# Optimization experiments

Hardware: AMD Instinct MI355X
Metric: run time of the kernel (lower is better)

The kernel has to match this reference:

```python
import jax, jax.numpy as jnp
import numpy as np

N, E, G = 8000, 32000, 256   # nodes, edges, graphs
F, H = 680, 10               # in-features, GAT heads
HF = F * H                   # 6800


def setup_inputs() -> dict:
    key = jax.random.key(0)
    ks = jax.random.split(key, 12)
    s = lambda i, shape, sc: (jax.random.normal(ks[i], shape, jnp.float32) * sc)
    x = jax.random.normal(ks[0], (N, F), jnp.float32)
    edge_index = jax.random.randint(ks[1], (2, E), 0, N)
    batch = jnp.arange(N) // (N // G)   # contiguous, every graph non-empty
    return dict(
        x=x, edge_index=edge_index, batch=batch,
        W_gat=s(2, (F, HF), 0.05), a_src=s(3, (H, F), 0.05), a_dst=s(4, (H, F), 0.05),
        b_gat=jnp.zeros((HF,), jnp.float32),
        W_gcn=s(5, (HF, HF), 0.01), b_gcn=jnp.zeros((HF,), jnp.float32),
        W1=s(6, (2 * HF, 512), 0.02), b1=jnp.zeros((512,), jnp.float32),
        W2=s(7, (512, 128), 0.05), b2=jnp.zeros((128,), jnp.float32),
        W3=s(8, (128, 64), 0.05), b3=jnp.zeros((64,), jnp.float32),
    )


def _self_loops(edge_index):
    loop = jnp.arange(N)
    return (jnp.concatenate([edge_index[0], loop]),
            jnp.concatenate([edge_index[1], loop]))


def _gat(x, src, dst, W, a_s, a_d, b):
    xh = (x @ W).reshape(N, H, F)                          # [N,H,F]
    al_s = jnp.einsum('nhf,hf->nh', xh, a_s)               # src attention logits
    al_d = jnp.einsum('nhf,hf->nh', xh, a_d)
    e = jax.nn.leaky_relu(al_s[src] + al_d[dst], 0.2)      # [Etot,H]
    m = jax.ops.segment_max(e, dst, num_segments=N)        # segment softmax over dst
    ex = jnp.exp(e - m[dst])
    z = jax.ops.segment_sum(ex, dst, num_segments=N)
    alpha = ex / (z[dst] + 1e-16)
    out = jax.ops.segment_sum(alpha[:, :, None] * xh[src], dst, num_segments=N)
    return out.reshape(N, HF) + b                          # concat heads + bias


def _gcn(x, src, dst, W, b):
    deg = jax.ops.segment_sum(jnp.ones_like(dst, jnp.float32), dst, num_segments=N)
    dinv = jax.lax.rsqrt(deg)                              # deg>=1 due to self-loops
    norm = dinv[src] * dinv[dst]
    xw = x @ W
    return jax.ops.segment_sum(norm[:, None] * xw[src], dst, num_segments=N) + b


def reference(x, edge_index, batch, W_gat, a_src, a_dst, b_gat, W_gcn, b_gcn,
              W1, b1, W2, b2, W3, b3):
    src, dst = _self_loops(edge_index)
    h = jax.nn.relu(_gat(x, src, dst, W_gat, a_src, a_dst, b_gat))  # dropout = id (eval)
    h = jax.nn.relu(_gcn(h, src, dst, W_gcn, b_gcn))
    gmp = jax.ops.segment_max(h, batch, num_segments=G)
    cnt = jax.ops.segment_sum(jnp.ones((N,), jnp.float32), batch, num_segments=G)
    gap = jax.ops.segment_sum(h, batch, num_segments=G) / cnt[:, None]
    g = jnp.concatenate([gmp, gap], axis=1)                # [G, 2*HF]
    g = jax.nn.relu(g @ W1 + b1)
    g = g @ W2 + b2
    return g @ W3 + b3                                     # [G, 64]
```

## Files before the change

kernel.cpp:

```cpp
#include <hip/hip_runtime.h>
#include <cstdint>
#include <cstddef>

#define DEVFN static __device__ __forceinline__

typedef __attribute__((ext_vector_type(8))) short short8;
typedef __attribute__((ext_vector_type(16))) float f32x16;

constexpr int NN  = 8000;
constexpr int NE  = 32000;
constexpr int ET  = NE + NN;
constexpr int NG  = 256;
constexpr int F   = 680;
constexpr int NH  = 10;
constexpr int HF  = 6800;

constexpr int MP   = 8192;
constexpr int KP1  = 704;
constexpr int NP   = 6912;
constexpr int KP2  = 6848;
constexpr int KM1P = 13632;

DEVFN unsigned short f2bf(float f) {
  unsigned u = __float_as_uint(f);
  u += 0x7fffu + ((u >> 16) & 1u);
  return (unsigned short)(u >> 16);
}
DEVFN float bf2f(unsigned short b) { return __uint_as_float(((unsigned)b) << 16); }

DEVFN int perm64(int k, int r) {
  return (((k >> 3) ^ (r & 7)) << 3) | (k & 7);
}

DEVFN void gload16(const void* g, void* l) {
  __builtin_amdgcn_global_load_lds(
      (const __attribute__((address_space(1))) unsigned int*)g,
      (__attribute__((address_space(3))) unsigned int*)l, 16, 0, 0);
}

DEVFN f32x16 mfma32(short8 a, short8 b, f32x16 c) {
  asm("v_mfma_f32_32x32x16_bf16 %0, %1, %2, %0" : "+v"(c) : "v"(a), "v"(b));
  return c;
}

template<int OUT_MODE, bool BIAS, bool RELU, bool SWZ>
__global__ __launch_bounds__(512, 2) void gemm256(
    const unsigned short* __restrict__ A, const unsigned short* __restrict__ BT,
    void* __restrict__ C, const float* __restrict__ bias,
    int K, int cstride, int nvalid, int Mt, int KC) {
  __shared__ alignas(16) char Lds[131072];
  const int tid = threadIdx.x;
  const int wave = tid >> 6, lane = tid & 63;
  const int wm = wave >> 2, wn = wave & 3;
  const int l31 = lane & 31, hi = lane >> 5, l7 = lane & 7;
  const int brow = (wn & 1) * 64;

  int bm, bn;
  if (SWZ) {
    const int xcd = blockIdx.x & 7;
    const int j = blockIdx.x >> 3;
    bm = j & 31;
    bn = (j >> 5) * 8 + xcd;
    const int Nt = (nvalid + 255) >> 8;
    if (bn >= Nt) return;
  } else {
    bm = blockIdx.x % Mt;
    bn = blockIdx.x / Mt;
  }

  const int NTt = K >> 6;
  const int kb = blockIdx.z * KC;
  const int NT = min(KC, NTt - kb);
  const unsigned short* Ag = A + (size_t)bm * 256 * K + (size_t)kb * 64;
  const unsigned short* Bg = BT + (size_t)bn * 256 * K + (size_t)kb * 64;

  const int srow = tid >> 3;
  const int schk = (tid & 7) * 8;

  auto stageHalf = [&](const unsigned short* G, int t, int op, int h) {
    char* base = Lds + ((((t & 1) << 2) | (op << 1) | h) << 14) + (wave << 10);
    const unsigned short* src = G + (size_t)(h * 128 + srow) * K + (size_t)t * 64 + schk;
    gload16(src, base);
    gload16(src + (size_t)64 * K, base + 8192);
  };
  auto stageTile = [&](int t) {
    stageHalf(Ag, t, 0, 0); stageHalf(Ag, t, 0, 1);
    stageHalf(Bg, t, 1, 0); stageHalf(Bg, t, 1, 1);
  };

  const char* Ab0 = Lds + (((0 << 2) | (0 << 1) | wm) << 14);
  const char* Ab1 = Lds + (((1 << 2) | (0 << 1) | wm) << 14);
  const char* Bb0 = Lds + (((0 << 2) | (1 << 1) | (wn >> 1)) << 14);
  const char* Bb1 = Lds + (((1 << 2) | (1 << 1) | (wn >> 1)) << 14);

  const int aoff = l31 * 128;
  const int boff = (brow + l31) * 128;

  f32x16 acc[4][2];
#pragma unroll
  for (int i = 0; i < 4; i++)
#pragma unroll
    for (int j = 0; j < 2; j++) acc[i][j] = (f32x16)(0.f);

  short8 a0[4], a1[4], b0v[2], b1v[2];

#define RD_A(DST, ABASE, KS) do {                                               \
  _Pragma("unroll") for (int m = 0; m < 4; ++m)                                 \
    DST[m] = *(const short8*)((ABASE) + m * 4096 + aoff                         \
                              + (((2 * (KS) + hi) ^ l7) << 4));                 \
} while (0)

#define RD_B(DST, BBASE, KS) do {                                               \
  _Pragma("unroll") for (int n = 0; n < 2; ++n)                                 \
    DST[n] = *(const short8*)((BBASE) + n * 4096 + boff                         \
                              + (((2 * (KS) + hi) ^ l7) << 4));                 \
} while (0)

#define MM(ASET, BSET) do {                                                     \
  __builtin_amdgcn_s_setprio(1);                                                \
  _Pragma("unroll") for (int m = 0; m < 4; ++m)                                 \
  _Pragma("unroll") for (int n = 0; n < 2; ++n)                                 \
    acc[m][n] = mfma32(ASET[m], BSET[n], acc[m][n]);                            \
  __builtin_amdgcn_s_setprio(0);                                                \
} while (0)

  if (NT > 1) {
    stageTile(0); stageTile(1);
    asm volatile("s_waitcnt vmcnt(8)" ::: "memory");
  } else {
    stageTile(0);
    asm volatile("s_waitcnt vmcnt(0)" ::: "memory");
  }
  asm volatile("s_barrier" ::: "memory");
  RD_A(a0, Ab0, 0); RD_B(b0v, Bb0, 0);

  for (int t = 0; t < NT; ++t) {
    const char* Ac = (t & 1) ? Ab1 : Ab0;
    const char* Bc = (t & 1) ? Bb1 : Bb0;
    const char* An = (t & 1) ? Ab0 : Ab1;
    const char* Bn = (t & 1) ? Bb0 : Bb1;

    RD_A(a1, Ac, 1); RD_B(b1v, Bc, 1);
    MM(a0, b0v);
    RD_A(a0, Ac, 2); RD_B(b0v, Bc, 2);
    MM(a1, b1v);
    RD_A(a1, Ac, 3); RD_B(b1v, Bc, 3);
    MM(a0, b0v);
    asm volatile("s_waitcnt lgkmcnt(0)" ::: "memory");
    asm volatile("s_barrier" ::: "memory");
    if (t + 2 < NT) {
      stageTile(t + 2);
      asm volatile("s_waitcnt vmcnt(8)" ::: "memory");
    } else if (t + 1 < NT) {
      asm volatile("s_waitcnt vmcnt(0)" ::: "memory");
    }
    if (t + 1 < NT) {
      asm volatile("s_barrier" ::: "memory");
      RD_A(a0, An, 0); RD_B(b0v, Bn, 0);
    }
    MM(a1, b1v);
  }

#undef RD_A
#undef RD_B
#undef MM

  const int m0 = bm * 256 + wm * 128;
  const int n0 = bn * 256 + wn * 64;
#pragma unroll
  for (int mf = 0; mf < 4; ++mf) {
#pragma unroll
    for (int nf = 0; nf < 2; ++nf) {
      int c = n0 + nf * 32 + l31;
      if (c >= nvalid) continue;
      float bv = BIAS ? bias[c] : 0.f;
#pragma unroll
      for (int reg = 0; reg < 16; ++reg) {
        int r = m0 + mf * 32 + (reg & 3) + 8 * (reg >> 2) + 4 * hi;
        float v = acc[mf][nf][reg] + bv;
        if (RELU) v = fmaxf(v, 0.f);
        if (OUT_MODE == 0) {
          ((float*)C)[(size_t)r * cstride + c] = v;
        } else if (OUT_MODE == 1) {
          ((unsigned short*)C)[(size_t)r * cstride + c] = f2bf(v);
        } else if (OUT_MODE == 2) {
          int pos = (c & ~63) + perm64(c & 63, r);
          ((unsigned short*)C)[(size_t)r * cstride + pos] = f2bf(v);
        } else {
          ((float*)C)[(size_t)blockIdx.z * (Mt * 256) * cstride + (size_t)r * cstride + c] = v;
        }
      }
    }
  }
}

template<bool RELU>
__global__ void finish_kernel(const float* __restrict__ acc, const float* __restrict__ bias,
                              unsigned short* __restrict__ out, int S, int M, int N) {
  int idx = blockIdx.x * 256 + threadIdx.x;
  if (idx >= M * N) return;
  int r = idx / N, c = idx - r * N;
  float s = bias[c];
  for (int k = 0; k < S; k++) s += acc[(size_t)k * M * N + (size_t)r * N + c];
  if (RELU) s = fmaxf(s, 0.f);
  out[(size_t)r * N + (c & ~63) + perm64(c & 63, r)] = f2bf(s);
}

__global__ void conv_x_kernel(const float* __restrict__ x, unsigned short* __restrict__ out) {
  int idx = blockIdx.x * 256 + threadIdx.x;
  constexpr int GR = KP1 / 4;
  if (idx >= MP * GR) return;
  int row = idx / GR, k = (idx - row * GR) * 4;
  unsigned short v[4] = {0, 0, 0, 0};
  if (row < NN && k < F) {
    const float* p = x + (size_t)row * F + k;
    v[0] = f2bf(p[0]); v[1] = f2bf(p[1]); v[2] = f2bf(p[2]); v[3] = f2bf(p[3]);
  }
  int pos = (k & ~63) + perm64(k & 63, row);
  uint2 pk;
  pk.x = (unsigned)v[0] | ((unsigned)v[1] << 16);
  pk.y = (unsigned)v[2] | ((unsigned)v[3] << 16);
  *(uint2*)&out[(size_t)row * KP1 + pos] = pk;
}

__global__ void convT_kernel(const float* __restrict__ in, unsigned short* __restrict__ out,
                             int K, int N, int KPad, int NPad) {
  __shared__ float tile[32][33];
  int n0 = blockIdx.x * 32, k0 = blockIdx.y * 32;
  int tx = threadIdx.x, ty = threadIdx.y;
#pragma unroll
  for (int i = 0; i < 4; i++) {
    int k = k0 + ty + i * 8, n = n0 + tx;
    tile[ty + i * 8][tx] = (k < K && n < N) ? in[(size_t)k * N + n] : 0.f;
  }
  __syncthreads();
#pragma unroll
  for (int i = 0; i < 4; i++) {
    int n = n0 + ty + i * 8, k = k0 + tx;
    if (n < NPad && k < KPad) {
      int pos = (k & ~63) + perm64(k & 63, n);
      out[(size_t)n * KPad + pos] = f2bf(tile[tx][ty + i * 8]);
    }
  }
}

__global__ void logits_kernel(const unsigned short* __restrict__ xh,
                              const float* __restrict__ a_src, const float* __restrict__ a_dst,
                              float* __restrict__ al_s, float* __restrict__ al_d) {
  int wid = blockIdx.x * 4 + (threadIdx.x >> 6);
  int lane = threadIdx.x & 63;
  int n = wid / NH, h = wid - n * NH;
  if (n >= NN) return;
  const unsigned short* row = xh + (size_t)n * NP + h * F;
  const float* as = a_src + h * F;
  const float* ad = a_dst + h * F;
  float ss = 0.f, sd = 0.f;
  for (int f0 = lane; f0 < F; f0 += 64) {
    float v = bf2f(row[f0]);
    ss += v * as[f0]; sd += v * ad[f0];
  }
#pragma unroll
  for (int o = 32; o > 0; o >>= 1) { ss += __shfl_down(ss, o); sd += __shfl_down(sd, o); }
  if (lane == 0) { al_s[wid] = ss; al_d[wid] = sd; }
}

__global__ void edge_count_kernel(const int* __restrict__ ei, int* __restrict__ deg) {
  int e = blockIdx.x * 256 + threadIdx.x;
  if (e >= ET) return;
  int d = (e < NE) ? ei[NE + e] : (e - NE);
  atomicAdd(&deg[d], 1);
}

__global__ void scan_kernel(const int* __restrict__ deg, int* __restrict__ rs,
                            int* __restrict__ cursor) {
  __shared__ int part[1024];
  int t = threadIdx.x;
  int base = t * 8, s = 0, loc[8];
#pragma unroll
  for (int i = 0; i < 8; i++) { loc[i] = s; int idx = base + i; s += (idx < NN) ? deg[idx] : 0; }
  part[t] = s;
  __syncthreads();
  for (int off = 1; off < 1024; off <<= 1) {
    int v = (t >= off) ? part[t - off] : 0;
    __syncthreads();
    part[t] += v;
    __syncthreads();
  }
  int pre = (t > 0) ? part[t - 1] : 0;
#pragma unroll
  for (int i = 0; i < 8; i++) {
    int idx = base + i;
    if (idx <= NN) { rs[idx] = pre + loc[i]; cursor[idx] = pre + loc[i]; }
  }
}

__global__ void edge_fill_kernel(const int* __restrict__ ei, int* __restrict__ cursor,
                                 int* __restrict__ eidx) {
  int e = blockIdx.x * 256 + threadIdx.x;
  if (e >= ET) return;
  int d = (e < NE) ? ei[NE + e] : (e - NE);
  int pos = atomicAdd(&cursor[d], 1);
  eidx[pos] = e;
}

__global__ void dinv_kernel(const int* __restrict__ deg, float* __restrict__ dinv) {
  int n = blockIdx.x * 256 + threadIdx.x;
  if (n < NN) dinv[n] = rsqrtf((float)max(deg[n], 1));
}

__global__ void alpha_kernel(const int* __restrict__ ei, const int* __restrict__ rs,
                             const int* __restrict__ eidx, const float* __restrict__ al_s,
                             const float* __restrict__ al_d, float* __restrict__ alpha) {
  int w = blockIdx.x * 256 + threadIdx.x;
  if (w >= NN * NH) return;
  int n = w / NH, h = w - n * NH;
  int s0 = rs[n], s1 = rs[n + 1];
  float ad = al_d[w];
  float m = -3.0e38f;
  for (int i = s0; i < s1; i++) {
    int e = eidx[i]; int s = (e < NE) ? ei[e] : (e - NE);
    float x = al_s[s * NH + h] + ad;
    x = (x > 0.f) ? x : 0.2f * x;
    m = fmaxf(m, x);
  }
  float z = 0.f;
  for (int i = s0; i < s1; i++) {
    int e = eidx[i]; int s = (e < NE) ? ei[e] : (e - NE);
    float x = al_s[s * NH + h] + ad;
    x = (x > 0.f) ? x : 0.2f * x;
    float ex = __expf(x - m);
    alpha[(size_t)i * NH + h] = ex;
    z += ex;
  }
  float inv = 1.f / (z + 1e-16f);
  for (int i = s0; i < s1; i++) alpha[(size_t)i * NH + h] *= inv;
}

DEVFN void axpy8(float al, uint4 r, float* a) {
  a[0] += al * bf2f((unsigned short)(r.x & 0xffff));
  a[1] += al * bf2f((unsigned short)(r.x >> 16));
  a[2] += al * bf2f((unsigned short)(r.y & 0xffff));
  a[3] += al * bf2f((unsigned short)(r.y >> 16));
  a[4] += al * bf2f((unsigned short)(r.z & 0xffff));
  a[5] += al * bf2f((unsigned short)(r.z >> 16));
  a[6] += al * bf2f((unsigned short)(r.w & 0xffff));
  a[7] += al * bf2f((unsigned short)(r.w >> 16));
}
DEVFN uint4 pack8(const float* a) {
  uint4 p;
  p.x = (unsigned)f2bf(a[0]) | ((unsigned)f2bf(a[1]) << 16);
  p.y = (unsigned)f2bf(a[2]) | ((unsigned)f2bf(a[3]) << 16);
  p.z = (unsigned)f2bf(a[4]) | ((unsigned)f2bf(a[5]) << 16);
  p.w = (unsigned)f2bf(a[6]) | ((unsigned)f2bf(a[7]) << 16);
  return p;
}

constexpr int MAXE = 256;

__global__ __launch_bounds__(256) void gat_agg_kernel(
    const unsigned short* __restrict__ xh, const int* __restrict__ ei,
    const int* __restrict__ rs, const int* __restrict__ eidx,
    const float* __restrict__ alpha, const float* __restrict__ bgat,
    unsigned short* __restrict__ hbf) {
  __shared__ int   Ls[MAXE];
  __shared__ float La[MAXE][NH];
  int n = blockIdx.x, t = threadIdx.x;
  int s0 = rs[n], d = rs[n + 1] - s0;
  int dc = min(d, MAXE);
  for (int i = t; i < dc; i += 256) {
    int e = eidx[s0 + i]; Ls[i] = (e < NE) ? ei[e] : (e - NE);
  }
  for (int j = t; j < dc * NH; j += 256)
    La[j / NH][j % NH] = alpha[(size_t)(s0 + j / NH) * NH + j % NH];
  __syncthreads();
  for (int c8 = t; c8 < KP2 / 8; c8 += 256) {
    int c = c8 * 8;
    int pos = (c & ~63) + ((((c >> 3) & 7) ^ (n & 7)) << 3);
    if (c >= HF) {
      *(uint4*)&hbf[(size_t)n * KP2 + pos] = make_uint4(0u, 0u, 0u, 0u);
      continue;
    }
    int h = c / F;
    float a[8] = {0.f, 0.f, 0.f, 0.f, 0.f, 0.f, 0.f, 0.f};
    for (int i = 0; i < dc; ++i)
      axpy8(La[i][h], *(const uint4*)&xh[(size_t)Ls[i] * NP + c], a);
    for (int i = MAXE; i < d; ++i) {
      int e = eidx[s0 + i]; int s = (e < NE) ? ei[e] : (e - NE);
      axpy8(alpha[(size_t)(s0 + i) * NH + h], *(const uint4*)&xh[(size_t)s * NP + c], a);
    }
#pragma unroll
    for (int q = 0; q < 8; ++q) a[q] = fmaxf(a[q] + bgat[c + q], 0.f);
    *(uint4*)&hbf[(size_t)n * KP2 + pos] = pack8(a);
  }
}

__global__ __launch_bounds__(256) void gcn_agg_kernel(
    const unsigned short* __restrict__ xw, const int* __restrict__ ei,
    const int* __restrict__ rs, const int* __restrict__ eidx,
    const float* __restrict__ dinv, const float* __restrict__ bgcn,
    unsigned short* __restrict__ h2) {
  __shared__ int   Ls[MAXE];
  __shared__ float Lw[MAXE];
  int n = blockIdx.x, t = threadIdx.x;
  int s0 = rs[n], d = rs[n + 1] - s0;
  int dc = min(d, MAXE);
  float dn = dinv[n];
  for (int i = t; i < dc; i += 256) {
    int e = eidx[s0 + i]; int s = (e < NE) ? ei[e] : (e - NE);
    Ls[i] = s; Lw[i] = dinv[s] * dn;
  }
  __syncthreads();
  for (int c8 = t; c8 < HF / 8; c8 += 256) {
    int c = c8 * 8;
    float a[8] = {0.f, 0.f, 0.f, 0.f, 0.f, 0.f, 0.f, 0.f};
    for (int i = 0; i < dc; ++i)
      axpy8(Lw[i], *(const uint4*)&xw[(size_t)Ls[i] * NP + c], a);
    for (int i = MAXE; i < d; ++i) {
      int e = eidx[s0 + i]; int s = (e < NE) ? ei[e] : (e - NE);
      axpy8(dinv[s] * dn, *(const uint4*)&xw[(size_t)s * NP + c], a);
    }
#pragma unroll
    for (int q = 0; q < 8; ++q) a[q] = fmaxf(a[q] + bgcn[c + q], 0.f);
    *(uint4*)&h2[(size_t)n * KP2 + c] = pack8(a);
  }
}

__global__ void pool_init_kernel(int* gstart, int* gend, int* gcnt) {
  int g = threadIdx.x;
  gstart[g] = 0x7fffffff; gend[g] = 0; gcnt[g] = 0;
}
__global__ void pool_scan_kernel(const int* __restrict__ batch, int* gstart, int* gend, int* gcnt) {
  int n = blockIdx.x * 256 + threadIdx.x;
  if (n >= NN) return;
  int b = batch[n];
  if (b >= 0 && b < NG) {
    atomicMin(&gstart[b], n);
    atomicMax(&gend[b], n + 1);
    atomicAdd(&gcnt[b], 1);
  }
}
__global__ void pool_kernel(const unsigned short* __restrict__ h2,
                            const int* __restrict__ gstart, const int* __restrict__ gend,
                            const int* __restrict__ gcnt, unsigned short* __restrict__ gbf) {
  int g = blockIdx.x, t = threadIdx.x;
  int s = gstart[g], e = gend[g];
  float inv = 1.f / (float)max(gcnt[g], 1);
  for (int c8 = t; c8 < HF / 8; c8 += 256) {
    int c = c8 * 8;
    float mx[8], sm[8];
#pragma unroll
    for (int q = 0; q < 8; ++q) { mx[q] = -3.0e38f; sm[q] = 0.f; }
    for (int n = s; n < e; ++n) {
      uint4 r = *(const uint4*)&h2[(size_t)n * KP2 + c];
      float v[8];
      v[0] = bf2f((unsigned short)(r.x & 0xffff)); v[1] = bf2f((unsigned short)(r.x >> 16));
      v[2] = bf2f((unsigned short)(r.y & 0xffff)); v[3] = bf2f((unsigned short)(r.y >> 16));
      v[4] = bf2f((unsigned short)(r.z & 0xffff)); v[5] = bf2f((unsigned short)(r.z >> 16));
      v[6] = bf2f((unsigned short)(r.w & 0xffff)); v[7] = bf2f((unsigned short)(r.w >> 16));
#pragma unroll
      for (int q = 0; q < 8; ++q) { mx[q] = fmaxf(mx[q], v[q]); sm[q] += v[q]; }
    }
#pragma unroll
    for (int q = 0; q < 8; ++q) sm[q] *= inv;
    int c2 = HF + c;
    int pos1 = (c & ~63) + ((((c >> 3) & 7) ^ (g & 7)) << 3);
    int pos2 = (c2 & ~63) + ((((c2 >> 3) & 7) ^ (g & 7)) << 3);
    *(uint4*)&gbf[(size_t)g * KM1P + pos1] = pack8(mx);
    *(uint4*)&gbf[(size_t)g * KM1P + pos2] = pack8(sm);
  }
}

extern "C" void kernel_launch(void* const* d_in, const int* in_sizes, int n_in,
                              void* d_out, int out_size, void* d_ws, size_t ws_size,
                              hipStream_t stream) {
  (void)in_sizes; (void)n_in; (void)out_size; (void)ws_size;
  const float* x     = (const float*)d_in[0];
  const int*   ei    = (const int*)d_in[1];
  const int*   batch = (const int*)d_in[2];
  const float* W_gat = (const float*)d_in[3];
  const float* a_src = (const float*)d_in[4];
  const float* a_dst = (const float*)d_in[5];
  const float* b_gat = (const float*)d_in[6];
  const float* W_gcn = (const float*)d_in[7];
  const float* b_gcn = (const float*)d_in[8];
  const float* W1    = (const float*)d_in[9];
  const float* b1    = (const float*)d_in[10];
  const float* W2    = (const float*)d_in[11];
  const float* b2    = (const float*)d_in[12];
  const float* W3    = (const float*)d_in[13];
  const float* b3    = (const float*)d_in[14];
  float* out = (float*)d_out;

  char* ws = (char*)d_ws;
  size_t off = 0;
  auto alloc = [&](size_t bytes) -> void* {
    void* p = ws + off;
    off += (bytes + 255) & ~(size_t)255;
    return p;
  };
  unsigned short* bufA  = (unsigned short*)alloc((size_t)MP * NP * 2);
  unsigned short* bufB  = (unsigned short*)alloc((size_t)MP * KP2 * 2);
  unsigned short* wgcnT = (unsigned short*)alloc((size_t)NP * KP2 * 2);
  unsigned short* xbf   = (unsigned short*)alloc((size_t)MP * KP1 * 2);
  unsigned short* wgatT = (unsigned short*)alloc((size_t)NP * KP1 * 2);
  unsigned short* w1T   = (unsigned short*)alloc((size_t)512 * KM1P * 2);
  unsigned short* gbf   = (unsigned short*)alloc((size_t)NG * KM1P * 2);
  unsigned short* w2T   = (unsigned short*)alloc((size_t)256 * 512 * 2);
  unsigned short* w3T   = (unsigned short*)alloc((size_t)256 * 128 * 2);
  unsigned short* g1bf  = (unsigned short*)alloc((size_t)NG * 512 * 2);
  unsigned short* g2bf  = (unsigned short*)alloc((size_t)NG * 128 * 2);
  float* accf  = (float*)alloc((size_t)8 * 256 * 512 * 4);
  float* al_s  = (float*)alloc((size_t)NN * NH * 4);
  float* al_d  = (float*)alloc((size_t)NN * NH * 4);
  float* alpha = (float*)alloc((size_t)ET * NH * 4);
  float* dinv  = (float*)alloc((size_t)NN * 4);
  int* deg    = (int*)alloc((size_t)NN * 4);
  int* rs     = (int*)alloc((size_t)(NN + 1) * 4);
  int* cursor = (int*)alloc((size_t)(NN + 1) * 4);
  int* eidx   = (int*)alloc((size_t)ET * 4);
  int* gstart = (int*)alloc((size_t)NG * 4);
  int* gend   = (int*)alloc((size_t)NG * 4);
  int* gcnt   = (int*)alloc((size_t)NG * 4);

  constexpr int MT = MP / 256;
  constexpr int GRID_SWZ = 32 * 32;

  conv_x_kernel<<<(MP * (KP1 / 4)) / 256, 256, 0, stream>>>(x, xbf);
  convT_kernel<<<dim3(NP / 32, KP1 / 32), dim3(32, 8), 0, stream>>>(W_gat, wgatT, F, HF, KP1, NP);
  convT_kernel<<<dim3(NP / 32, KP2 / 32), dim3(32, 8), 0, stream>>>(W_gcn, wgcnT, HF, HF, KP2, NP);
  convT_kernel<<<dim3(512 / 32, KM1P / 32), dim3(32, 8), 0, stream>>>(W1, w1T, 2 * HF, 512, KM1P, 512);
  convT_kernel<<<dim3(256 / 32, 512 / 32), dim3(32, 8), 0, stream>>>(W2, w2T, 512, 128, 512, 256);
  convT_kernel<<<dim3(256 / 32, 128 / 32), dim3(32, 8), 0, stream>>>(W3, w3T, 128, 64, 128, 256);
  hipMemsetAsync(deg, 0, (size_t)NN * 4, stream);
  hipMemsetAsync((char*)bufB + (size_t)NN * KP2 * 2, 0, (size_t)(MP - NN) * KP2 * 2, stream);
  hipMemsetAsync(gbf, 0, (size_t)NG * KM1P * 2, stream);

  gemm256<1, false, false, true><<<dim3(GRID_SWZ, 1, 1), 512, 0, stream>>>(
      xbf, wgatT, bufA, nullptr, KP1, NP, NP, MT, KP1 / 64);

  logits_kernel<<<(NN * NH) / 4, 256, 0, stream>>>(bufA, a_src, a_dst, al_s, al_d);

  edge_count_kernel<<<(ET + 255) / 256, 256, 0, stream>>>(ei, deg);
  scan_kernel<<<1, 1024, 0, stream>>>(deg, rs, cursor);
  edge_fill_kernel<<<(ET + 255) / 256, 256, 0, stream>>>(ei, cursor, eidx);
  dinv_kernel<<<(NN + 255) / 256, 256, 0, stream>>>(deg, dinv);

  alpha_kernel<<<(NN * NH + 255) / 256, 256, 0, stream>>>(ei, rs, eidx, al_s, al_d, alpha);

  gat_agg_kernel<<<NN, 256, 0, stream>>>(bufA, ei, rs, eidx, alpha, b_gat, bufB);

  gemm256<1, false, false, true><<<dim3(GRID_SWZ, 1, 1), 512, 0, stream>>>(
      bufB, wgcnT, bufA, nullptr, KP2, NP, NP, MT, KP2 / 64);

  gcn_agg_kernel<<<NN, 256, 0, stream>>>(bufA, ei, rs, eidx, dinv, b_gcn, bufB);

  pool_init_kernel<<<1, 256, 0, stream>>>(gstart, gend, gcnt);
  pool_scan_kernel<<<(NN + 255) / 256, 256, 0, stream>>>(batch, gstart, gend, gcnt);
  pool_kernel<<<NG, 256, 0, stream>>>(bufB, gstart, gend, gcnt, gbf);

  gemm256<3, false, false, false><<<dim3(1 * 2, 1, 8), 512, 0, stream>>>(
      gbf, w1T, accf, nullptr, KM1P, 512, 512, 1, 27);
  finish_kernel<true><<<(256 * 512) / 256, 256, 0, stream>>>(accf, b1, g1bf, 8, 256, 512);

  gemm256<3, false, false, false><<<dim3(1, 1, 4), 512, 0, stream>>>(
      g1bf, w2T, accf, nullptr, 512, 128, 128, 1, 2);
  finish_kernel<false><<<(256 * 128) / 256, 256, 0, stream>>>(accf, b2, g2bf, 4, 256, 128);

  gemm256<0, true, false, false><<<dim3(1, 1, 1), 512, 0, stream>>>(
      g2bf, w3T, out, b3, 128, 64, 64, 1, 2);
}
```

Measured before the change: 1.422 ms.

## Switch GEMM to 128x256 tiles with 16x16x32 MFMA and deeper split-K

The bf16 GEMM kernel moves from 256x256 block tiles built on 32x32x16 MFMAs to 128x256 tiles built on 16x16x32 MFMAs. LDS use drops from 128KB to 96KB, the swizzled grid doubles the number of M tiles, and the main loop interleaves LDS reads, MFMAs and global-to-LDS prefetch differently. The small MLP GEMMs now use more split-K slices (31 instead of 8) to fill more CUs. The aim is better occupancy and load balance, at the cost of less operand reuse per tile and more partial-sum traffic in the finish step.

```diff
diff --git a/kernel.cpp b/kernel.cpp
--- a/kernel.cpp
+++ b/kernel.cpp
@@ -5,7 +5,7 @@
 #define DEVFN static __device__ __forceinline__
 
 typedef __attribute__((ext_vector_type(8))) short short8;
-typedef __attribute__((ext_vector_type(16))) float f32x16;
+typedef __attribute__((ext_vector_type(4))) float f32x4;
 
 constexpr int NN  = 8000;
 constexpr int NE  = 32000;
@@ -38,8 +38,8 @@
       (__attribute__((address_space(3))) unsigned int*)l, 16, 0, 0);
 }
 
-DEVFN f32x16 mfma32(short8 a, short8 b, f32x16 c) {
-  asm("v_mfma_f32_32x32x16_bf16 %0, %1, %2, %0" : "+v"(c) : "v"(a), "v"(b));
+DEVFN f32x4 mfma16(short8 a, short8 b, f32x4 c) {
+  asm("v_mfma_f32_16x16x32_bf16 %0, %1, %2, %0" : "+v"(c) : "v"(a), "v"(b));
   return c;
 }
 
@@ -48,19 +48,18 @@
     const unsigned short* __restrict__ A, const unsigned short* __restrict__ BT,
     void* __restrict__ C, const float* __restrict__ bias,
     int K, int cstride, int nvalid, int Mt, int KC) {
-  __shared__ alignas(16) char Lds[131072];
+  __shared__ alignas(16) char Lds[98304];
   const int tid = threadIdx.x;
   const int wave = tid >> 6, lane = tid & 63;
   const int wm = wave >> 2, wn = wave & 3;
-  const int l31 = lane & 31, hi = lane >> 5, l7 = lane & 7;
-  const int brow = (wn & 1) * 64;
+  const int g4 = lane >> 4, l15 = lane & 15, l7 = lane & 7;
 
   int bm, bn;
   if (SWZ) {
     const int xcd = blockIdx.x & 7;
     const int j = blockIdx.x >> 3;
-    bm = j & 31;
-    bn = (j >> 5) * 8 + xcd;
+    bm = j & 63;
+    bn = (j >> 6) * 8 + xcd;
     const int Nt = (nvalid + 255) >> 8;
     if (bn >= Nt) return;
   } else {
@@ -71,113 +70,107 @@
   const int NTt = K >> 6;
   const int kb = blockIdx.z * KC;
   const int NT = min(KC, NTt - kb);
-  const unsigned short* Ag = A + (size_t)bm * 256 * K + (size_t)kb * 64;
+  const unsigned short* Ag = A + (size_t)bm * 128 * K + (size_t)kb * 64;
   const unsigned short* Bg = BT + (size_t)bn * 256 * K + (size_t)kb * 64;
 
-  const int srow = tid >> 3;
-  const int schk = (tid & 7) * 8;
-
-  auto stageHalf = [&](const unsigned short* G, int t, int op, int h) {
-    char* base = Lds + ((((t & 1) << 2) | (op << 1) | h) << 14) + (wave << 10);
-    const unsigned short* src = G + (size_t)(h * 128 + srow) * K + (size_t)t * 64 + schk;
+  const size_t soff = (size_t)(tid >> 3) * K + (size_t)(tid & 7) * 8;
+
+  auto stageA = [&](int t) {
+    char* base = Lds + (t & 1) * 49152 + (wave << 10);
+    const unsigned short* src = Ag + soff + (size_t)t * 64;
     gload16(src, base);
     gload16(src + (size_t)64 * K, base + 8192);
   };
-  auto stageTile = [&](int t) {
-    stageHalf(Ag, t, 0, 0); stageHalf(Ag, t, 0, 1);
-    stageHalf(Bg, t, 1, 0); stageHalf(Bg, t, 1, 1);
+  auto stageB = [&](int t) {
+    char* base = Lds + (t & 1) * 49152 + 16384 + (wave << 10);
+    const unsigned short* src = Bg + soff + (size_t)t * 64;
+    gload16(src, base);
+    gload16(src + (size_t)64 * K, base + 8192);
+    gload16(src + (size_t)128 * K, base + 16384);
+    gload16(src + (size_t)192 * K, base + 24576);
   };
 
-  const char* Ab0 = Lds + (((0 << 2) | (0 << 1) | wm) << 14);
-  const char* Ab1 = Lds + (((1 << 2) | (0 << 1) | wm) << 14);
-  const char* Bb0 = Lds + (((0 << 2) | (1 << 1) | (wn >> 1)) << 14);
-  const char* Bb1 = Lds + (((1 << 2) | (1 << 1) | (wn >> 1)) << 14);
-
-  const int aoff = l31 * 128;
-  const int boff = (brow + l31) * 128;
-
-  f32x16 acc[4][2];
+  f32x4 acc[4][4];
 #pragma unroll
   for (int i = 0; i < 4; i++)
 #pragma unroll
-    for (int j = 0; j < 2; j++) acc[i][j] = (f32x16)(0.f);
-
-  short8 a0[4], a1[4], b0v[2], b1v[2];
-
-#define RD_A(DST, ABASE, KS) do {                                               \
-  _Pragma("unroll") for (int m = 0; m < 4; ++m)                                 \
-    DST[m] = *(const short8*)((ABASE) + m * 4096 + aoff                         \
-                              + (((2 * (KS) + hi) ^ l7) << 4));                 \
+    for (int j = 0; j < 4; j++) acc[i][j] = (f32x4){0.f, 0.f, 0.f, 0.f};
+
+  short8 aR[2][2][2], bR[2][2][2];
+
+#define RD_A(MH, AB) do {                                                        \
+  _Pragma("unroll") for (int i2 = 0; i2 < 2; ++i2)                               \
+  _Pragma("unroll") for (int ks = 0; ks < 2; ++ks)                               \
+    aR[MH][i2][ks] = *(const short8*)((AB) + (wm * 64 + ((MH) * 2 + i2) * 16 + l15) * 128 \
+                                      + ((((ks << 2) | g4) ^ l7) << 4));          \
 } while (0)
 
-#define RD_B(DST, BBASE, KS) do {                                               \
-  _Pragma("unroll") for (int n = 0; n < 2; ++n)                                 \
-    DST[n] = *(const short8*)((BBASE) + n * 4096 + boff                         \
-                              + (((2 * (KS) + hi) ^ l7) << 4));                 \
+#define RD_B(NH, BB) do {                                                        \
+  _Pragma("unroll") for (int j2 = 0; j2 < 2; ++j2)                               \
+  _Pragma("unroll") for (int ks = 0; ks < 2; ++ks)                               \
+    bR[NH][j2][ks] = *(const short8*)((BB) + (wn * 64 + ((NH) * 2 + j2) * 16 + l15) * 128 \
+                                      + ((((ks << 2) | g4) ^ l7) << 4));          \
 } while (0)
 
-#define MM(ASET, BSET) do {                                                     \
-  __builtin_amdgcn_s_setprio(1);                                                \
-  _Pragma("unroll") for (int m = 0; m < 4; ++m)                                 \
-  _Pragma("unroll") for (int n = 0; n < 2; ++n)                                 \
-    acc[m][n] = mfma32(ASET[m], BSET[n], acc[m][n]);                            \
-  __builtin_amdgcn_s_setprio(0);                                                \
+#define MM(MH, NH) do {                                                          \
+  __builtin_amdgcn_s_setprio(1);                                                 \
+  _Pragma("unroll") for (int i2 = 0; i2 < 2; ++i2)                               \
+  _Pragma("unroll") for (int j2 = 0; j2 < 2; ++j2)                               \
+  _Pragma("unroll") for (int ks = 0; ks < 2; ++ks)                               \
+    acc[(MH) * 2 + i2][(NH) * 2 + j2] =                                          \
+        mfma16(aR[MH][i2][ks], bR[NH][j2][ks], acc[(MH) * 2 + i2][(NH) * 2 + j2]); \
+  __builtin_amdgcn_s_setprio(0);                                                 \
 } while (0)
 
+  stageA(0); stageB(0);
   if (NT > 1) {
-    stageTile(0); stageTile(1);
-    asm volatile("s_waitcnt vmcnt(8)" ::: "memory");
+    stageA(1); stageB(1);
+    asm volatile("s_waitcnt vmcnt(6)" ::: "memory");
   } else {
-    stageTile(0);
     asm volatile("s_waitcnt vmcnt(0)" ::: "memory");
   }
   asm volatile("s_barrier" ::: "memory");
-  RD_A(a0, Ab0, 0); RD_B(b0v, Bb0, 0);
 
   for (int t = 0; t < NT; ++t) {
-    const char* Ac = (t & 1) ? Ab1 : Ab0;
-    const char* Bc = (t & 1) ? Bb1 : Bb0;
-    const char* An = (t & 1) ? Ab0 : Ab1;
-    const char* Bn = (t & 1) ? Bb0 : Bb1;
-
-    RD_A(a1, Ac, 1); RD_B(b1v, Bc, 1);
-    MM(a0, b0v);
-    RD_A(a0, Ac, 2); RD_B(b0v, Bc, 2);
-    MM(a1, b1v);
-    RD_A(a1, Ac, 3); RD_B(b1v, Bc, 3);
-    MM(a0, b0v);
-    asm volatile("s_waitcnt lgkmcnt(0)" ::: "memory");
+    const char* Ab = Lds + (t & 1) * 49152;
+    const char* Bb = Ab + 16384;
+    const bool pf = (t + 2 < NT);
+
+    RD_A(0, Ab);
+    RD_B(0, Bb);
+    RD_B(1, Bb);
+    MM(0, 0);
+    RD_A(1, Ab);
+    MM(0, 1);
     asm volatile("s_barrier" ::: "memory");
-    if (t + 2 < NT) {
-      stageTile(t + 2);
-      asm volatile("s_waitcnt vmcnt(8)" ::: "memory");
-    } else if (t + 1 < NT) {
-      asm volatile("s_waitcnt vmcnt(0)" ::: "memory");
-    }
-    if (t + 1 < NT) {
-      asm volatile("s_barrier" ::: "memory");
-      RD_A(a0, An, 0); RD_B(b0v, Bn, 0);
-    }
-    MM(a1, b1v);
+    if (pf) stageB(t + 2);
+    MM(1, 1);
+    asm volatile("s_barrier" ::: "memory");
+    if (pf) stageA(t + 2);
+    MM(1, 0);
+    if (pf) asm volatile("s_waitcnt vmcnt(6)" ::: "memory");
+    else    asm volatile("s_waitcnt vmcnt(0)" ::: "memory");
+    asm volatile("s_barrier" ::: "memory");
   }
 
 #undef RD_A
 #undef RD_B
 #undef MM
 
-  const int m0 = bm * 256 + wm * 128;
+  const int m0 = bm * 128 + wm * 64;
   const int n0 = bn * 256 + wn * 64;
-#pragma unroll
-  for (int mf = 0; mf < 4; ++mf) {
-#pragma unroll
-    for (int nf = 0; nf < 2; ++nf) {
-      int c = n0 + nf * 32 + l31;
+  const int rb = g4 * 4;
+#pragma unroll
+  for (int i = 0; i < 4; i++) {
+#pragma unroll
+    for (int j = 0; j < 4; j++) {
+      int c = n0 + j * 16 + l15;
       if (c >= nvalid) continue;
       float bv = BIAS ? bias[c] : 0.f;
 #pragma unroll
-      for (int reg = 0; reg < 16; ++reg) {
-        int r = m0 + mf * 32 + (reg & 3) + 8 * (reg >> 2) + 4 * hi;
-        float v = acc[mf][nf][reg] + bv;
+      for (int tt = 0; tt < 4; tt++) {
+        int r = m0 + i * 16 + rb + tt;
+        float v = acc[i][j][tt] + bv;
         if (RELU) v = fmaxf(v, 0.f);
         if (OUT_MODE == 0) {
           ((float*)C)[(size_t)r * cstride + c] = v;
@@ -187,7 +180,7 @@
           int pos = (c & ~63) + perm64(c & 63, r);
           ((unsigned short*)C)[(size_t)r * cstride + pos] = f2bf(v);
         } else {
-          ((float*)C)[(size_t)blockIdx.z * (Mt * 256) * cstride + (size_t)r * cstride + c] = v;
+          ((float*)C)[(size_t)blockIdx.z * (Mt * 128) * cstride + (size_t)r * cstride + c] = v;
         }
       }
     }
@@ -509,7 +502,7 @@
   unsigned short* w3T   = (unsigned short*)alloc((size_t)256 * 128 * 2);
   unsigned short* g1bf  = (unsigned short*)alloc((size_t)NG * 512 * 2);
   unsigned short* g2bf  = (unsigned short*)alloc((size_t)NG * 128 * 2);
-  float* accf  = (float*)alloc((size_t)8 * 256 * 512 * 4);
+  float* accf  = (float*)alloc((size_t)32 * 256 * 512 * 4);
   float* al_s  = (float*)alloc((size_t)NN * NH * 4);
   float* al_d  = (float*)alloc((size_t)NN * NH * 4);
   float* alpha = (float*)alloc((size_t)ET * NH * 4);
@@ -522,8 +515,7 @@
   int* gend   = (int*)alloc((size_t)NG * 4);
   int* gcnt   = (int*)alloc((size_t)NG * 4);
 
-  constexpr int MT = MP / 256;
-  constexpr int GRID_SWZ = 32 * 32;
+  constexpr int GRID_SWZ = 8 * 64 * 4;
 
   conv_x_kernel<<<(MP * (KP1 / 4)) / 256, 256, 0, stream>>>(x, xbf);
   convT_kernel<<<dim3(NP / 32, KP1 / 32), dim3(32, 8), 0, stream>>>(W_gat, wgatT, F, HF, KP1, NP);
@@ -536,7 +528,7 @@
   hipMemsetAsync(gbf, 0, (size_t)NG * KM1P * 2, stream);
 
   gemm256<1, false, false, true><<<dim3(GRID_SWZ, 1, 1), 512, 0, stream>>>(
-      xbf, wgatT, bufA, nullptr, KP1, NP, NP, MT, KP1 / 64);
+      xbf, wgatT, bufA, nullptr, KP1, NP, NP, 64, KP1 / 64);
 
   logits_kernel<<<(NN * NH) / 4, 256, 0, stream>>>(bufA, a_src, a_dst, al_s, al_d);
 
@@ -550,7 +542,7 @@
   gat_agg_kernel<<<NN, 256, 0, stream>>>(bufA, ei, rs, eidx, alpha, b_gat, bufB);
 
   gemm256<1, false, false, true><<<dim3(GRID_SWZ, 1, 1), 512, 0, stream>>>(
-      bufB, wgcnT, bufA, nullptr, KP2, NP, NP, MT, KP2 / 64);
+      bufB, wgcnT, bufA, nullptr, KP2, NP, NP, 64, KP2 / 64);
 
   gcn_agg_kernel<<<NN, 256, 0, stream>>>(bufA, ei, rs, eidx, dinv, b_gcn, bufB);
 
@@ -558,14 +550,14 @@
   pool_scan_kernel<<<(NN + 255) / 256, 256, 0, stream>>>(batch, gstart, gend, gcnt);
   pool_kernel<<<NG, 256, 0, stream>>>(bufB, gstart, gend, gcnt, gbf);
 
-  gemm256<3, false, false, false><<<dim3(1 * 2, 1, 8), 512, 0, stream>>>(
-      gbf, w1T, accf, nullptr, KM1P, 512, 512, 1, 27);
-  finish_kernel<true><<<(256 * 512) / 256, 256, 0, stream>>>(accf, b1, g1bf, 8, 256, 512);
-
-  gemm256<3, false, false, false><<<dim3(1, 1, 4), 512, 0, stream>>>(
-      g1bf, w2T, accf, nullptr, 512, 128, 128, 1, 2);
+  gemm256<3, false, false, false><<<dim3(2 * 2, 1, 31), 512, 0, stream>>>(
+      gbf, w1T, accf, nullptr, KM1P, 512, 512, 2, 7);
+  finish_kernel<true><<<(256 * 512) / 256, 256, 0, stream>>>(accf, b1, g1bf, 31, 256, 512);
+
+  gemm256<3, false, false, false><<<dim3(2, 1, 4), 512, 0, stream>>>(
+      g1bf, w2T, accf, nullptr, 512, 128, 128, 2, 2);
   finish_kernel<false><<<(256 * 128) / 256, 256, 0, stream>>>(accf, b2, g2bf, 4, 256, 128);
 
-  gemm256<0, true, false, false><<<dim3(1, 1, 1), 512, 0, stream>>>(
-      g2bf, w3T, out, b3, 128, 64, 64, 1, 2);
-}
+  gemm256<0, true, false, false><<<dim3(2, 1, 1), 512, 0, stream>>>(
+      g2bf, w3T, out, b3, 128, 64, 64, 2, 2);
+}
```

Result: slower. 1.491 ms (+4.9%).

## Switch GEMM to 16x16x32 MFMA with quadrant-staged LDS reads and deeper split-K

Applied to the files above, without the earlier changes.

Replaces the 32x32x16 bf16 MFMA tiles with 16x16x32 tiles arranged as four quadrants per wave. LDS fragment reads are interleaved with MFMA issue, and the last quadrant's MFMAs are deferred into the next K iteration. This aims to overlap LDS loads with compute and shorten the dependency stalls. The W1 GEMM also goes from 8-way to 31-way split-K for more parallelism, at the cost of a larger partial-sum buffer and more reduction work in finish_kernel.

```diff
diff --git a/kernel.cpp b/kernel.cpp
--- a/kernel.cpp
+++ b/kernel.cpp
@@ -5,7 +5,7 @@
 #define DEVFN static __device__ __forceinline__
 
 typedef __attribute__((ext_vector_type(8))) short short8;
-typedef __attribute__((ext_vector_type(16))) float f32x16;
+typedef __attribute__((ext_vector_type(4))) float f32x4;
 
 constexpr int NN  = 8000;
 constexpr int NE  = 32000;
@@ -38,8 +38,8 @@
       (__attribute__((address_space(3))) unsigned int*)l, 16, 0, 0);
 }
 
-DEVFN f32x16 mfma32(short8 a, short8 b, f32x16 c) {
-  asm("v_mfma_f32_32x32x16_bf16 %0, %1, %2, %0" : "+v"(c) : "v"(a), "v"(b));
+DEVFN f32x4 mfma16(short8 a, short8 b, f32x4 c) {
+  asm("v_mfma_f32_16x16x32_bf16 %0, %1, %2, %0" : "+v"(c) : "v"(a), "v"(b));
   return c;
 }
 
@@ -52,7 +52,7 @@
   const int tid = threadIdx.x;
   const int wave = tid >> 6, lane = tid & 63;
   const int wm = wave >> 2, wn = wave & 3;
-  const int l31 = lane & 31, hi = lane >> 5, l7 = lane & 7;
+  const int g4 = lane >> 4, l15 = lane & 15, l7 = lane & 7;
   const int brow = (wn & 1) * 64;
 
   int bm, bn;
@@ -93,59 +93,61 @@
   const char* Bb0 = Lds + (((0 << 2) | (1 << 1) | (wn >> 1)) << 14);
   const char* Bb1 = Lds + (((1 << 2) | (1 << 1) | (wn >> 1)) << 14);
 
-  const int aoff = l31 * 128;
-  const int boff = (brow + l31) * 128;
-
-  f32x16 acc[4][2];
-#pragma unroll
-  for (int i = 0; i < 4; i++)
-#pragma unroll
-    for (int j = 0; j < 2; j++) acc[i][j] = (f32x16)(0.f);
-
-  short8 a0[4], a1[4], b0v[2], b1v[2];
-
-#define RD_A(DST, ABASE, KS) do {                                               \
-  _Pragma("unroll") for (int m = 0; m < 4; ++m)                                 \
-    DST[m] = *(const short8*)((ABASE) + m * 4096 + aoff                         \
-                              + (((2 * (KS) + hi) ^ l7) << 4));                 \
+  f32x4 acc[8][4];
+#pragma unroll
+  for (int i = 0; i < 8; i++)
+#pragma unroll
+    for (int j = 0; j < 4; j++) acc[i][j] = (f32x4){0.f, 0.f, 0.f, 0.f};
+
+  short8 aQ0[4][2], aQ1[4][2], bL[2][2], bH[2][2];
+
+#define RD_AQ(DST, BASE, QM) do {                                                \
+  _Pragma("unroll") for (int i2 = 0; i2 < 4; ++i2)                               \
+  _Pragma("unroll") for (int ks = 0; ks < 2; ++ks)                               \
+    DST[i2][ks] = *(const short8*)((BASE) + ((QM) * 64 + i2 * 16 + l15) * 128    \
+                                   + ((((ks << 2) | g4) ^ l7) << 4));            \
 } while (0)
 
-#define RD_B(DST, BBASE, KS) do {                                               \
-  _Pragma("unroll") for (int n = 0; n < 2; ++n)                                 \
-    DST[n] = *(const short8*)((BBASE) + n * 4096 + boff                         \
-                              + (((2 * (KS) + hi) ^ l7) << 4));                 \
+#define RD_BQ(DST, BASE, QN) do {                                               \
+  _Pragma("unroll") for (int j2 = 0; j2 < 2; ++j2)                              \
+  _Pragma("unroll") for (int ks = 0; ks < 2; ++ks)                              \
+    DST[j2][ks] = *(const short8*)((BASE) + (brow + (QN) * 32 + j2 * 16 + l15) * 128 \
+                                   + ((((ks << 2) | g4) ^ l7) << 4));           \
 } while (0)
 
-#define MM(ASET, BSET) do {                                                     \
+#define MMQ(QM, QN, ASET, BSET) do {                                            \
   __builtin_amdgcn_s_setprio(1);                                                \
-  _Pragma("unroll") for (int m = 0; m < 4; ++m)                                 \
-  _Pragma("unroll") for (int n = 0; n < 2; ++n)                                 \
-    acc[m][n] = mfma32(ASET[m], BSET[n], acc[m][n]);                            \
+  _Pragma("unroll") for (int i2 = 0; i2 < 4; ++i2)                              \
+  _Pragma("unroll") for (int j2 = 0; j2 < 2; ++j2)                              \
+  _Pragma("unroll") for (int ks = 0; ks < 2; ++ks)                              \
+    acc[(QM) * 4 + i2][(QN) * 2 + j2] =                                         \
+        mfma16(ASET[i2][ks], BSET[j2][ks], acc[(QM) * 4 + i2][(QN) * 2 + j2]);  \
   __builtin_amdgcn_s_setprio(0);                                                \
 } while (0)
 
+  stageTile(0);
   if (NT > 1) {
-    stageTile(0); stageTile(1);
+    stageTile(1);
     asm volatile("s_waitcnt vmcnt(8)" ::: "memory");
   } else {
-    stageTile(0);
     asm volatile("s_waitcnt vmcnt(0)" ::: "memory");
   }
   asm volatile("s_barrier" ::: "memory");
-  RD_A(a0, Ab0, 0); RD_B(b0v, Bb0, 0);
+  RD_AQ(aQ0, Ab0, 0);
 
   for (int t = 0; t < NT; ++t) {
     const char* Ac = (t & 1) ? Ab1 : Ab0;
     const char* Bc = (t & 1) ? Bb1 : Bb0;
-    const char* An = (t & 1) ? Ab0 : Ab1;
-    const char* Bn = (t & 1) ? Bb0 : Bb1;
-
-    RD_A(a1, Ac, 1); RD_B(b1v, Bc, 1);
-    MM(a0, b0v);
-    RD_A(a0, Ac, 2); RD_B(b0v, Bc, 2);
-    MM(a1, b1v);
-    RD_A(a1, Ac, 3); RD_B(b1v, Bc, 3);
-    MM(a0, b0v);
+
+    if (t > 0) {
+      MMQ(1, 1, aQ1, bH);
+      MMQ(1, 0, aQ1, bL);
+    }
+    RD_BQ(bL, Bc, 0);
+    RD_BQ(bH, Bc, 1);
+    MMQ(0, 0, aQ0, bL);
+    RD_AQ(aQ1, Ac, 1);
+    MMQ(0, 1, aQ0, bH);
     asm volatile("s_waitcnt lgkmcnt(0)" ::: "memory");
     asm volatile("s_barrier" ::: "memory");
     if (t + 2 < NT) {
@@ -156,28 +158,31 @@
     }
     if (t + 1 < NT) {
       asm volatile("s_barrier" ::: "memory");
-      RD_A(a0, An, 0); RD_B(b0v, Bn, 0);
-    }
-    MM(a1, b1v);
-  }
-
-#undef RD_A
-#undef RD_B
-#undef MM
+      const char* An = (t & 1) ? Ab0 : Ab1;
+      RD_AQ(aQ0, An, 0);
+    }
+  }
+  MMQ(1, 1, aQ1, bH);
+  MMQ(1, 0, aQ1, bL);
+
+#undef RD_AQ
+#undef RD_BQ
+#undef MMQ
 
   const int m0 = bm * 256 + wm * 128;
   const int n0 = bn * 256 + wn * 64;
-#pragma unroll
-  for (int mf = 0; mf < 4; ++mf) {
-#pragma unroll
-    for (int nf = 0; nf < 2; ++nf) {
-      int c = n0 + nf * 32 + l31;
+  const int rb = g4 * 4;
+#pragma unroll
+  for (int i = 0; i < 8; i++) {
+#pragma unroll
+    for (int j = 0; j < 4; j++) {
+      int c = n0 + j * 16 + l15;
       if (c >= nvalid) continue;
       float bv = BIAS ? bias[c] : 0.f;
 #pragma unroll
-      for (int reg = 0; reg < 16; ++reg) {
-        int r = m0 + mf * 32 + (reg & 3) + 8 * (reg >> 2) + 4 * hi;
-        float v = acc[mf][nf][reg] + bv;
+      for (int tt = 0; tt < 4; tt++) {
+        int r = m0 + i * 16 + rb + tt;
+        float v = acc[i][j][tt] + bv;
         if (RELU) v = fmaxf(v, 0.f);
         if (OUT_MODE == 0) {
           ((float*)C)[(size_t)r * cstride + c] = v;
@@ -509,7 +514,7 @@
   unsigned short* w3T   = (unsigned short*)alloc((size_t)256 * 128 * 2);
   unsigned short* g1bf  = (unsigned short*)alloc((size_t)NG * 512 * 2);
   unsigned short* g2bf  = (unsigned short*)alloc((size_t)NG * 128 * 2);
-  float* accf  = (float*)alloc((size_t)8 * 256 * 512 * 4);
+  float* accf  = (float*)alloc((size_t)32 * 256 * 512 * 4);
   float* al_s  = (float*)alloc((size_t)NN * NH * 4);
   float* al_d  = (float*)alloc((size_t)NN * NH * 4);
   float* alpha = (float*)alloc((size_t)ET * NH * 4);
@@ -522,8 +527,7 @@
   int* gend   = (int*)alloc((size_t)NG * 4);
   int* gcnt   = (int*)alloc((size_t)NG * 4);
 
-  constexpr int MT = MP / 256;
-  constexpr int GRID_SWZ = 32 * 32;
+  constexpr int GRID_SWZ = 8 * 32 * 4;
 
   conv_x_kernel<<<(MP * (KP1 / 4)) / 256, 256, 0, stream>>>(x, xbf);
   convT_kernel<<<dim3(NP / 32, KP1 / 32), dim3(32, 8), 0, stream>>>(W_gat, wgatT, F, HF, KP1, NP);
@@ -536,7 +540,7 @@
   hipMemsetAsync(gbf, 0, (size_t)NG * KM1P * 2, stream);
 
   gemm256<1, false, false, true><<<dim3(GRID_SWZ, 1, 1), 512, 0, stream>>>(
-      xbf, wgatT, bufA, nullptr, KP1, NP, NP, MT, KP1 / 64);
+      xbf, wgatT, bufA, nullptr, KP1, NP, NP, 32, KP1 / 64);
 
   logits_kernel<<<(NN * NH) / 4, 256, 0, stream>>>(bufA, a_src, a_dst, al_s, al_d);
 
@@ -550,7 +554,7 @@
   gat_agg_kernel<<<NN, 256, 0, stream>>>(bufA, ei, rs, eidx, alpha, b_gat, bufB);
 
   gemm256<1, false, false, true><<<dim3(GRID_SWZ, 1, 1), 512, 0, stream>>>(
-      bufB, wgcnT, bufA, nullptr, KP2, NP, NP, MT, KP2 / 64);
+      bufB, wgcnT, bufA, nullptr, KP2, NP, NP, 32, KP2 / 64);
 
   gcn_agg_kernel<<<NN, 256, 0, stream>>>(bufA, ei, rs, eidx, dinv, b_gcn, bufB);
 
@@ -558,9 +562,9 @@
   pool_scan_kernel<<<(NN + 255) / 256, 256, 0, stream>>>(batch, gstart, gend, gcnt);
   pool_kernel<<<NG, 256, 0, stream>>>(bufB, gstart, gend, gcnt, gbf);
 
-  gemm256<3, false, false, false><<<dim3(1 * 2, 1, 8), 512, 0, stream>>>(
-      gbf, w1T, accf, nullptr, KM1P, 512, 512, 1, 27);
-  finish_kernel<true><<<(256 * 512) / 256, 256, 0, stream>>>(accf, b1, g1bf, 8, 256, 512);
+  gemm256<3, false, false, false><<<dim3(2, 1, 31), 512, 0, stream>>>(
+      gbf, w1T, accf, nullptr, KM1P, 512, 512, 1, 7);
+  finish_kernel<true><<<(256 * 512) / 256, 256, 0, stream>>>(accf, b1, g1bf, 31, 256, 512);
 
   gemm256<3, false, false, false><<<dim3(1, 1, 4), 512, 0, stream>>>(
       g1bf, w2T, accf, nullptr, 512, 128, 128, 1, 2);
```

Result: faster. 1.366 ms (-3.9%).
